# Optimization experiments

Measured on AMD Instinct MI355X. Metric: run time of the kernel, lower is better.

The kernel has to match this reference:

```python
import jax, jax.numpy as jnp
import numpy as np

B, S, H_DIM = 2, 2048, 1024
N_HEADS, HEAD_DIM = 16, 64
EPS = 1e-6


def phi(x):
    return jax.nn.elu(x) + 1.0


def setup_inputs() -> dict:
    key = jax.random.key(0)
    ks = jax.random.split(key, 11)
    std = 0.02
    proj = N_HEADS * HEAD_DIM
    return {
        "query": jax.random.normal(ks[0], (B, S, H_DIM), dtype=jnp.float32),
        "key": jax.random.normal(ks[1], (B, S, H_DIM), dtype=jnp.float32),
        "value": jax.random.normal(ks[2], (B, S, H_DIM), dtype=jnp.float32),
        "Wq": jax.random.normal(ks[3], (proj, H_DIM), dtype=jnp.float32) * std,
        "bq": jnp.zeros((proj,), dtype=jnp.float32),
        "Wk": jax.random.normal(ks[4], (proj, H_DIM), dtype=jnp.float32) * std,
        "bk": jnp.zeros((proj,), dtype=jnp.float32),
        "Wv": jax.random.normal(ks[5], (proj, H_DIM), dtype=jnp.float32) * std,
        "bv": jnp.zeros((proj,), dtype=jnp.float32),
        "Wo": jax.random.normal(ks[6], (H_DIM, proj), dtype=jnp.float32) * std,
        "bo": jnp.zeros((H_DIM,), dtype=jnp.float32),
    }


def reference(query, key, value, Wq, bq, Wk, bk, Wv, bv, Wo, bo):
    b, s, _ = query.shape
    # QKV projections (torch nn.Linear: y = x @ W.T + b)
    q = query @ Wq.T + bq
    k = key @ Wk.T + bk
    v = value @ Wv.T + bv
    # (b, s, h*d) -> (b, h, s, d)
    def split_heads(t):
        return t.reshape(b, s, N_HEADS, HEAD_DIM).transpose(0, 2, 1, 3)
    q, k, v = split_heads(q), split_heads(k), split_heads(v)

    q_phi = phi(q)  # (b,h,s,d)
    k_phi = phi(k)

    # cumulative outer products: (b,h,s,d_k,d_v)
    kv = k_phi[..., :, None] * v[..., None, :]
    kv_cumsum = jnp.cumsum(kv, axis=2)
    k_phi_cumsum = jnp.cumsum(k_phi, axis=2)

    out_num = jnp.einsum('bhsd,bhsdj->bhsj', q_phi, kv_cumsum)
    out_den = jnp.einsum('bhsd,bhsd->bhs', q_phi, k_phi_cumsum)
    out = out_num / (out_den[..., None] + EPS)

    out = out.transpose(0, 2, 1, 3).reshape(b, s, N_HEADS * HEAD_DIM)
    return out @ Wo.T + bo
```

## Files before the change

### kernel.cpp

```cpp
#include <hip/hip_runtime.h>
#include <hip/hip_bf16.h>
#include <stdint.h>

typedef __bf16 bf16x8 __attribute__((ext_vector_type(8)));
typedef float  f32x4  __attribute__((ext_vector_type(4)));
typedef __hip_bfloat16 hbf16;

#define AS1 __attribute__((address_space(1)))
#define AS3 __attribute__((address_space(3)))

__device__ __forceinline__ void gload_lds16(const void* g, void* l) {
  __builtin_amdgcn_global_load_lds((const AS1 void*)g, (AS3 void*)l, 16, 0, 0);
}

__device__ __forceinline__ f32x4 mfma_bf16(bf16x8 a, bf16x8 b, f32x4 c) {
  return __builtin_amdgcn_mfma_f32_16x16x32_bf16(a, b, c, 0, 0, 0);
}


__global__ __launch_bounds__(256) void convert_all(
    const float* __restrict__ q, const float* __restrict__ k, const float* __restrict__ v,
    const float* __restrict__ wq, const float* __restrict__ wk,
    const float* __restrict__ wv, const float* __restrict__ wo,
    hbf16* __restrict__ dst)
{
  const int i8 = (blockIdx.x * 256 + threadIdx.x) * 8;
  const float* src;
  int off;
  if      (i8 < (4  << 20)) { src = q;  off = i8; }
  else if (i8 < (8  << 20)) { src = k;  off = i8 - (4  << 20); }
  else if (i8 < (12 << 20)) { src = v;  off = i8 - (8  << 20); }
  else if (i8 < (13 << 20)) { src = wq; off = i8 - (12 << 20); }
  else if (i8 < (14 << 20)) { src = wk; off = i8 - (13 << 20); }
  else if (i8 < (15 << 20)) { src = wv; off = i8 - (14 << 20); }
  else                      { src = wo; off = i8 - (15 << 20); }
  const float4 a = *(const float4*)(src + off);
  const float4 b = *(const float4*)(src + off + 4);
  hbf16 h[8];
  h[0] = __float2bfloat16(a.x); h[1] = __float2bfloat16(a.y);
  h[2] = __float2bfloat16(a.z); h[3] = __float2bfloat16(a.w);
  h[4] = __float2bfloat16(b.x); h[5] = __float2bfloat16(b.y);
  h[6] = __float2bfloat16(b.z); h[7] = __float2bfloat16(b.w);
  *(uint4*)(dst + i8) = *(uint4*)h;
}

__device__ __forceinline__ void gemm_core_128(
    const hbf16* __restrict__ A, const hbf16* __restrict__ Bw,
    int by, int bx, hbf16* sA, hbf16* sB, f32x4 (&acc)[4][4])
{
  const int tid  = threadIdx.x;
  const int lane = tid & 63;
  const int wid  = tid >> 6;
  const int wm = wid >> 1, wn = wid & 1;
  const int l15 = lane & 15, l4 = lane >> 4;
  const int K = 1024;

  for (int kt = 0; kt < 16; ++kt) {
    if (kt) __syncthreads();
    const int k0 = kt * 64;
    #pragma unroll
    for (int j = 0; j < 4; ++j) {
      const int o   = (j * 256 + tid) * 16;
      const int row = o >> 7;
      const int csw = (o & 127) ^ ((row & 7) << 4);
      gload_lds16((const char*)A  + ((size_t)(by * 128 + row) * K + k0) * 2 + csw,
                  (char*)sA + o);
      gload_lds16((const char*)Bw + ((size_t)(bx * 128 + row) * K + k0) * 2 + csw,
                  (char*)sB + o);
    }
    asm volatile("s_waitcnt vmcnt(0)" ::: "memory");
    __syncthreads();
    #pragma unroll
    for (int kk = 0; kk < 2; ++kk) {
      bf16x8 af[4], bfr[4];
      #pragma unroll
      for (int m = 0; m < 4; ++m) {
        const int row = wm * 64 + m * 16 + l15;
        const int col = (kk * 64 + l4 * 16) ^ ((row & 7) << 4);
        af[m] = *(const bf16x8*)((const char*)sA + row * 128 + col);
      }
      #pragma unroll
      for (int n = 0; n < 4; ++n) {
        const int row = wn * 64 + n * 16 + l15;
        const int col = (kk * 64 + l4 * 16) ^ ((row & 7) << 4);
        bfr[n] = *(const bf16x8*)((const char*)sB + row * 128 + col);
      }
      #pragma unroll
      for (int m = 0; m < 4; ++m) {
        #pragma unroll
        for (int n = 0; n < 4; ++n) {
          acc[m][n] = mfma_bf16(af[m], bfr[n], acc[m][n]);
        }
      }
    }
  }
}

__global__ __launch_bounds__(256) void qkv_gemm(
    const hbf16* __restrict__ qin, const hbf16* __restrict__ kin, const hbf16* __restrict__ vin,
    const hbf16* __restrict__ wq, const hbf16* __restrict__ wk, const hbf16* __restrict__ wv,
    const float* __restrict__ bq, const float* __restrict__ bk, const float* __restrict__ bv,
    hbf16* __restrict__ q_phi, hbf16* __restrict__ k_phi,
    hbf16* __restrict__ kphiT, hbf16* __restrict__ vT)
{
  const int z = blockIdx.z;
  const hbf16* A    = (z == 0) ? qin : (z == 1) ? kin : vin;
  const hbf16* W    = (z == 0) ? wq  : (z == 1) ? wk  : wv;
  const float* bias = (z == 0) ? bq  : (z == 1) ? bk  : bv;

  __shared__ hbf16 sA[128 * 64];
  __shared__ hbf16 sB[128 * 64];
  f32x4 acc[4][4] = {};
  gemm_core_128(A, W, blockIdx.y, blockIdx.x, sA, sB, acc);

  const int tid = threadIdx.x, lane = tid & 63, wid = tid >> 6;
  const int wm = wid >> 1, wn = wid & 1, l15 = lane & 15, l4 = lane >> 4;

  #pragma unroll
  for (int n = 0; n < 4; ++n) {
    const int gn = blockIdx.x * 128 + wn * 64 + n * 16 + l15;
    const float bs = bias[gn];
    const int h = gn >> 6, dd = gn & 63;
    #pragma unroll
    for (int m = 0; m < 4; ++m) {
      #pragma unroll
      for (int j = 0; j < 4; ++j) {
        const int gm = blockIdx.y * 128 + wm * 64 + m * 16 + l4 * 4 + j;
        const int b = gm >> 11, s = gm & 2047;
        float val = acc[m][n][j] + bs;
        if (z < 2) val = (val > 0.f) ? (val + 1.f) : __expf(val);
        const hbf16 hv = __float2bfloat16(val);
        const int bh = b * 16 + h;
        if (z == 0) {
          q_phi[((size_t)bh * 2048 + s) * 64 + dd] = hv;
        } else if (z == 1) {
          k_phi[((size_t)bh * 2048 + s) * 64 + dd] = hv;
          kphiT[((size_t)bh * 32 + (s >> 6)) * 4096 + dd * 64 + (s & 63)] = hv;
        } else {
          vT[((size_t)bh * 32 + (s >> 6)) * 4096 + dd * 64 + (s & 63)] = hv;
        }
      }
    }
  }
}

__global__ __launch_bounds__(256) void chunk_sums(
    const hbf16* __restrict__ kphiT, const hbf16* __restrict__ vT,
    float* __restrict__ sums)
{
  const int c = blockIdx.x, bh = blockIdx.y;
  const int tid = threadIdx.x, lane = tid & 63, w = tid >> 6;
  const int l15 = lane & 15, l4 = lane >> 4;
  const size_t tbase = ((size_t)bh * 32 + c) * 4096;

  f32x4 acc[5] = {};
  #pragma unroll
  for (int kk = 0; kk < 2; ++kk) {
    const bf16x8 bfr = *(const bf16x8*)&kphiT[tbase + (w * 16 + l15) * 64 + l4 * 8 + kk * 32];
    #pragma unroll
    for (int mj = 0; mj < 5; ++mj) {
      bf16x8 af;
      if (mj < 4) {
        af = *(const bf16x8*)&vT[tbase + (mj * 16 + l15) * 64 + l4 * 8 + kk * 32];
      } else {
        const __bf16 e = (l15 == 0) ? (__bf16)1.0f : (__bf16)0.0f;
        #pragma unroll
        for (int i = 0; i < 8; ++i) af[i] = e;
      }
      acc[mj] = mfma_bf16(af, bfr, acc[mj]);
    }
  }
  float* outp = sums + ((size_t)bh * 32 + c) * 5120;
  #pragma unroll
  for (int mj = 0; mj < 5; ++mj) {
    #pragma unroll
    for (int j = 0; j < 4; ++j) {
      outp[(mj * 16 + l4 * 4 + j) * 64 + w * 16 + l15] = acc[mj][j];
    }
  }
}

__global__ __launch_bounds__(256) void chunk_scan(
    const float* __restrict__ sums, hbf16* __restrict__ pre)
{
  const int bh = blockIdx.x, tid = threadIdx.x;
  float st[20];
  #pragma unroll
  for (int e = 0; e < 20; ++e) st[e] = 0.f;
  for (int c = 0; c < 32; ++c) {
    const size_t base = ((size_t)bh * 32 + c) * 5120;
    #pragma unroll
    for (int e = 0; e < 20; ++e) {
      const int p = e * 256 + tid;
      pre[base + p] = __float2bfloat16(st[e]);
      st[e] += sums[base + p];
    }
  }
}

__global__ __launch_bounds__(256) void attn_chunk(
    const hbf16* __restrict__ q_phi, const hbf16* __restrict__ k_phi,
    const hbf16* __restrict__ vT, const hbf16* __restrict__ pre,
    hbf16* __restrict__ attn)
{
  const int c = blockIdx.x, bh = blockIdx.y;
  const int tid = threadIdx.x, lane = tid & 63, w = tid >> 6;
  const int l15 = lane & 15, l4 = lane >> 4;
  __shared__ hbf16 sS[4 * 16 * 64];

  const size_t qbase = ((size_t)bh * 2048 + c * 64) * 64;
  const size_t tbase = ((size_t)bh * 32 + c) * 4096;
  const size_t pbase = ((size_t)bh * 32 + c) * 5120;

  bf16x8 aq[2];
  #pragma unroll
  for (int kk = 0; kk < 2; ++kk)
    aq[kk] = *(const bf16x8*)&q_phi[qbase + (w * 16 + l15) * 64 + l4 * 8 + kk * 32];

  f32x4 accS[4] = {};
  #pragma unroll
  for (int kk = 0; kk < 2; ++kk) {
    #pragma unroll
    for (int ni = 0; ni < 4; ++ni) {
      const bf16x8 bk = *(const bf16x8*)&k_phi[qbase + (ni * 16 + l15) * 64 + l4 * 8 + kk * 32];
      accS[ni] = mfma_bf16(aq[kk], bk, accS[ni]);
    }
  }
  #pragma unroll
  for (int ni = 0; ni < 4; ++ni) {
    #pragma unroll
    for (int j = 0; j < 4; ++j) {
      const int r  = l4 * 4 + j;
      const int cc = ni * 16 + l15;
      const float v = (cc <= w * 16 + r) ? accS[ni][j] : 0.f;
      sS[w * 1024 + r * 64 + (cc ^ ((r & 7) << 3))] = __float2bfloat16(v);
    }
  }

  f32x4 accN[5] = {};
  #pragma unroll
  for (int kk = 0; kk < 2; ++kk) {
    const bf16x8 aS = *(const bf16x8*)&sS[w * 1024 + l15 * 64 +
                                          ((l4 * 8 + kk * 32) ^ ((l15 & 7) << 3))];
    #pragma unroll
    for (int ni = 0; ni < 5; ++ni) {
      bf16x8 bv;
      if (ni < 4) {
        bv = *(const bf16x8*)&vT[tbase + (ni * 16 + l15) * 64 + l4 * 8 + kk * 32];
      } else {
        const __bf16 e = (l15 == 0) ? (__bf16)1.0f : (__bf16)0.0f;
        #pragma unroll
        for (int i = 0; i < 8; ++i) bv[i] = e;
      }
      accN[ni] = mfma_bf16(aS, bv, accN[ni]);
    }
  }
  #pragma unroll
  for (int kk = 0; kk < 2; ++kk) {
    #pragma unroll
    for (int ni = 0; ni < 5; ++ni) {
      const bf16x8 bp = *(const bf16x8*)&pre[pbase + (ni * 16 + l15) * 64 + l4 * 8 + kk * 32];
      accN[ni] = mfma_bf16(aq[kk], bp, accN[ni]);
    }
  }
  const int b = bh >> 4, h = bh & 15;
  #pragma unroll
  for (int j = 0; j < 4; ++j) {
    const float den = __shfl(accN[4][j], lane & 48);
    const float inv = 1.f / (den + 1e-6f);
    const int sg = c * 64 + w * 16 + l4 * 4 + j;
    #pragma unroll
    for (int ni = 0; ni < 4; ++ni) {
      attn[((size_t)b * 2048 + sg) * 1024 + h * 64 + ni * 16 + l15] =
          __float2bfloat16(accN[ni][j] * inv);
    }
  }
}

__global__ __launch_bounds__(256) void out_gemm(
    const hbf16* __restrict__ attn, const hbf16* __restrict__ wo,
    const float* __restrict__ bo, float* __restrict__ out)
{
  __shared__ hbf16 sA[128 * 64];
  __shared__ hbf16 sB[128 * 64];
  f32x4 acc[4][4] = {};
  gemm_core_128(attn, wo, blockIdx.y, blockIdx.x, sA, sB, acc);

  const int tid = threadIdx.x, lane = tid & 63, wid = tid >> 6;
  const int wm = wid >> 1, wn = wid & 1, l15 = lane & 15, l4 = lane >> 4;
  #pragma unroll
  for (int n = 0; n < 4; ++n) {
    const int gn = blockIdx.x * 128 + wn * 64 + n * 16 + l15;
    const float bs = bo[gn];
    #pragma unroll
    for (int m = 0; m < 4; ++m) {
      #pragma unroll
      for (int j = 0; j < 4; ++j) {
        const int gm = blockIdx.y * 128 + wm * 64 + m * 16 + l4 * 4 + j;
        out[(size_t)gm * 1024 + gn] = acc[m][n][j] + bs;
      }
    }
  }
}

extern "C" void kernel_launch(void* const* d_in, const int* in_sizes, int n_in,
                              void* d_out, int out_size, void* d_ws, size_t ws_size,
                              hipStream_t stream) {
  const float* q  = (const float*)d_in[0];
  const float* k  = (const float*)d_in[1];
  const float* v  = (const float*)d_in[2];
  const float* Wq = (const float*)d_in[3];
  const float* bq = (const float*)d_in[4];
  const float* Wk = (const float*)d_in[5];
  const float* bk = (const float*)d_in[6];
  const float* Wv = (const float*)d_in[7];
  const float* bv = (const float*)d_in[8];
  const float* Wo = (const float*)d_in[9];
  const float* bo = (const float*)d_in[10];

  char* ws = (char*)d_ws;
  const size_t MB = (size_t)1 << 20;
  hbf16* qin  = (hbf16*)(ws + 0 * MB);
  hbf16* kin  = (hbf16*)(ws + 8 * MB);
  hbf16* vin  = (hbf16*)(ws + 16 * MB);
  hbf16* wqb  = (hbf16*)(ws + 24 * MB);
  hbf16* wkb  = (hbf16*)(ws + 26 * MB);
  hbf16* wvb  = (hbf16*)(ws + 28 * MB);
  hbf16* wob  = (hbf16*)(ws + 30 * MB);
  hbf16* qphi = (hbf16*)(ws + 32 * MB);
  hbf16* kphi = (hbf16*)(ws + 40 * MB);
  hbf16* kphT = (hbf16*)(ws + 48 * MB);
  hbf16* vTb  = (hbf16*)(ws + 56 * MB);
  hbf16* attn = (hbf16*)(ws + 64 * MB);
  float* sums = (float*)(ws + 72 * MB);
  hbf16* pre  = (hbf16*)(ws + 92 * MB);

  convert_all<<<8192, 256, 0, stream>>>(q, k, v, Wq, Wk, Wv, Wo, qin);
  qkv_gemm<<<dim3(8, 32, 3), 256, 0, stream>>>(qin, kin, vin, wqb, wkb, wvb,
                                               bq, bk, bv, qphi, kphi, kphT, vTb);
  chunk_sums<<<dim3(32, 32), 256, 0, stream>>>(kphT, vTb, sums);
  chunk_scan<<<32, 256, 0, stream>>>(sums, pre);
  attn_chunk<<<dim3(32, 32), 256, 0, stream>>>(qphi, kphi, vTb, pre, attn);
  out_gemm<<<dim3(8, 32), 256, 0, stream>>>(attn, wob, bo, (float*)d_out);
}
```

Baseline: 227.7 us.

## Overlap GEMM tile loads with MFMA, remap blocks, parallelize chunk scan

```diff
diff --git a/kernel.cpp b/kernel.cpp
--- a/kernel.cpp
+++ b/kernel.cpp
@@ -55,8 +55,7 @@
   const int l15 = lane & 15, l4 = lane >> 4;
   const int K = 1024;
 
-  for (int kt = 0; kt < 16; ++kt) {
-    if (kt) __syncthreads();
+  auto STAGE = [&](int kt) {
     const int k0 = kt * 64;
     #pragma unroll
     for (int j = 0; j < 4; ++j) {
@@ -68,35 +67,50 @@
       gload_lds16((const char*)Bw + ((size_t)(bx * 128 + row) * K + k0) * 2 + csw,
                   (char*)sB + o);
     }
-    asm volatile("s_waitcnt vmcnt(0)" ::: "memory");
+  };
+
+  STAGE(0);
+  for (int kt = 0; kt < 16; ++kt) {
     __syncthreads();
+    bf16x8 af[2][4], bfr[2][4];
     #pragma unroll
     for (int kk = 0; kk < 2; ++kk) {
-      bf16x8 af[4], bfr[4];
       #pragma unroll
       for (int m = 0; m < 4; ++m) {
         const int row = wm * 64 + m * 16 + l15;
         const int col = (kk * 64 + l4 * 16) ^ ((row & 7) << 4);
-        af[m] = *(const bf16x8*)((const char*)sA + row * 128 + col);
+        af[kk][m] = *(const bf16x8*)((const char*)sA + row * 128 + col);
       }
       #pragma unroll
       for (int n = 0; n < 4; ++n) {
         const int row = wn * 64 + n * 16 + l15;
         const int col = (kk * 64 + l4 * 16) ^ ((row & 7) << 4);
-        bfr[n] = *(const bf16x8*)((const char*)sB + row * 128 + col);
-      }
+        bfr[kk][n] = *(const bf16x8*)((const char*)sB + row * 128 + col);
+      }
+    }
+    __syncthreads();
+    if (kt < 15) STAGE(kt + 1);
+    __builtin_amdgcn_sched_barrier(0);
+    #pragma unroll
+    for (int kk = 0; kk < 2; ++kk) {
       #pragma unroll
       for (int m = 0; m < 4; ++m) {
         #pragma unroll
         for (int n = 0; n < 4; ++n) {
-          acc[m][n] = mfma_bf16(af[m], bfr[n], acc[m][n]);
+          acc[m][n] = mfma_bf16(af[kk][m], bfr[kk][n], acc[m][n]);
         }
       }
     }
   }
 }
 
-__global__ __launch_bounds__(256) void qkv_gemm(
+__device__ __forceinline__ void xcd_remap(int& bx, int& by) {
+  const int X = blockIdx.x, Y = blockIdx.y;
+  by = X * 4 + (Y & 3);
+  bx = Y >> 2;
+}
+
+__global__ __launch_bounds__(256, 3) void qkv_gemm(
     const hbf16* __restrict__ qin, const hbf16* __restrict__ kin, const hbf16* __restrict__ vin,
     const hbf16* __restrict__ wq, const hbf16* __restrict__ wk, const hbf16* __restrict__ wv,
     const float* __restrict__ bq, const float* __restrict__ bk, const float* __restrict__ bv,
@@ -108,24 +122,27 @@
   const hbf16* W    = (z == 0) ? wq  : (z == 1) ? wk  : wv;
   const float* bias = (z == 0) ? bq  : (z == 1) ? bk  : bv;
 
+  int bx, by;
+  xcd_remap(bx, by);
+
   __shared__ hbf16 sA[128 * 64];
   __shared__ hbf16 sB[128 * 64];
   f32x4 acc[4][4] = {};
-  gemm_core_128(A, W, blockIdx.y, blockIdx.x, sA, sB, acc);
+  gemm_core_128(A, W, by, bx, sA, sB, acc);
 
   const int tid = threadIdx.x, lane = tid & 63, wid = tid >> 6;
   const int wm = wid >> 1, wn = wid & 1, l15 = lane & 15, l4 = lane >> 4;
 
   #pragma unroll
   for (int n = 0; n < 4; ++n) {
-    const int gn = blockIdx.x * 128 + wn * 64 + n * 16 + l15;
+    const int gn = bx * 128 + wn * 64 + n * 16 + l15;
     const float bs = bias[gn];
     const int h = gn >> 6, dd = gn & 63;
     #pragma unroll
     for (int m = 0; m < 4; ++m) {
       #pragma unroll
       for (int j = 0; j < 4; ++j) {
-        const int gm = blockIdx.y * 128 + wm * 64 + m * 16 + l4 * 4 + j;
+        const int gm = by * 128 + wm * 64 + m * 16 + l4 * 4 + j;
         const int b = gm >> 11, s = gm & 2047;
         float val = acc[m][n][j] + bs;
         if (z < 2) val = (val > 0.f) ? (val + 1.f) : __expf(val);
@@ -183,18 +200,17 @@
 __global__ __launch_bounds__(256) void chunk_scan(
     const float* __restrict__ sums, hbf16* __restrict__ pre)
 {
-  const int bh = blockIdx.x, tid = threadIdx.x;
-  float st[20];
-  #pragma unroll
-  for (int e = 0; e < 20; ++e) st[e] = 0.f;
+  const int elem = blockIdx.x * 256 + threadIdx.x;
+  const int bh = blockIdx.y;
+  const size_t base = (size_t)bh * 32 * 5120 + elem;
+  float v[32];
+  #pragma unroll
+  for (int c = 0; c < 32; ++c) v[c] = sums[base + (size_t)c * 5120];
+  float run = 0.f;
+  #pragma unroll
   for (int c = 0; c < 32; ++c) {
-    const size_t base = ((size_t)bh * 32 + c) * 5120;
-    #pragma unroll
-    for (int e = 0; e < 20; ++e) {
-      const int p = e * 256 + tid;
-      pre[base + p] = __float2bfloat16(st[e]);
-      st[e] += sums[base + p];
-    }
+    pre[base + (size_t)c * 5120] = __float2bfloat16(run);
+    run += v[c];
   }
 }
 
@@ -277,26 +293,29 @@
   }
 }
 
-__global__ __launch_bounds__(256) void out_gemm(
+__global__ __launch_bounds__(256, 3) void out_gemm(
     const hbf16* __restrict__ attn, const hbf16* __restrict__ wo,
     const float* __restrict__ bo, float* __restrict__ out)
 {
+  int bx, by;
+  xcd_remap(bx, by);
+
   __shared__ hbf16 sA[128 * 64];
   __shared__ hbf16 sB[128 * 64];
   f32x4 acc[4][4] = {};
-  gemm_core_128(attn, wo, blockIdx.y, blockIdx.x, sA, sB, acc);
+  gemm_core_128(attn, wo, by, bx, sA, sB, acc);
 
   const int tid = threadIdx.x, lane = tid & 63, wid = tid >> 6;
   const int wm = wid >> 1, wn = wid & 1, l15 = lane & 15, l4 = lane >> 4;
   #pragma unroll
   for (int n = 0; n < 4; ++n) {
-    const int gn = blockIdx.x * 128 + wn * 64 + n * 16 + l15;
+    const int gn = bx * 128 + wn * 64 + n * 16 + l15;
     const float bs = bo[gn];
     #pragma unroll
     for (int m = 0; m < 4; ++m) {
       #pragma unroll
       for (int j = 0; j < 4; ++j) {
-        const int gm = blockIdx.y * 128 + wm * 64 + m * 16 + l4 * 4 + j;
+        const int gm = by * 128 + wm * 64 + m * 16 + l4 * 4 + j;
         out[(size_t)gm * 1024 + gn] = acc[m][n][j] + bs;
       }
     }
@@ -339,7 +358,7 @@
   qkv_gemm<<<dim3(8, 32, 3), 256, 0, stream>>>(qin, kin, vin, wqb, wkb, wvb,
                                                bq, bk, bv, qphi, kphi, kphT, vTb);
   chunk_sums<<<dim3(32, 32), 256, 0, stream>>>(kphT, vTb, sums);
-  chunk_scan<<<32, 256, 0, stream>>>(sums, pre);
+  chunk_scan<<<dim3(20, 32), 256, 0, stream>>>(sums, pre);
   attn_chunk<<<dim3(32, 32), 256, 0, stream>>>(qphi, kphi, vTb, pre, attn);
   out_gemm<<<dim3(8, 32), 256, 0, stream>>>(attn, wob, bo, (float*)d_out);
 }
```

Result: faster. 201.4 us (-11.6%).
